# Optimization experiments

Hardware: AMD Instinct MI355X
Metric: run time of the kernel (lower is better)

## Reference

```python
import jax, jax.numpy as jnp
import numpy as np
from functools import partial

ALPHA = 2.0  # surrogate sharpness

@partial(jax.custom_vjp, nondiff_argnums=(1,))
def spike(x, alpha):
    # Heaviside forward, atan surrogate backward
    return (x >= 0.0).astype(x.dtype)

def _spike_fwd(x, alpha):
    return spike(x, alpha), x

def _spike_bwd(alpha, x, g):
    grad = (alpha / 2.0) / (1.0 + (jnp.pi / 2.0 * alpha * x) ** 2)
    return (g * grad,)

spike.defvjp(_spike_fwd, _spike_bwd)


def setup_inputs() -> dict:
    key = jax.random.key(0)
    k1, k2, k3 = jax.random.split(key, 3)
    B, T, H = 128, 2048, 512
    TAU_INIT, TH_INIT = 8.0, 0.5
    x_seq = jax.random.normal(k1, (B, T, 2), dtype=jnp.float32)
    W_in = jax.random.normal(k2, (2, H), dtype=jnp.float32) * (1.0 / np.sqrt(2.0))
    b_in = jnp.zeros((H,), dtype=jnp.float32)
    # PLIF: sigmoid(w_tau) = 1/tau  =>  w_tau = -log(tau - 1)
    w_tau = jnp.full((H,), -np.log(TAU_INIT - 1.0), dtype=jnp.float32)
    threshold = jnp.full((H,), TH_INIT, dtype=jnp.float32)
    W_out = jax.random.normal(k3, (H, 2), dtype=jnp.float32) * (1.0 / np.sqrt(H))
    b_out = jnp.zeros((2,), dtype=jnp.float32)
    return {"x_seq": x_seq, "W_in": W_in, "b_in": b_in,
            "w_tau": w_tau, "threshold": threshold,
            "W_out": W_out, "b_out": b_out}


def reference(x_seq, W_in, b_in, w_tau, threshold, W_out, b_out):
    B, T, _ = x_seq.shape
    H = W_in.shape[1]
    cur = x_seq @ W_in + b_in                      # [B, T, H]
    decay = jax.nn.sigmoid(w_tau)                  # [H], = 1/tau

    def step(v, c):
        v = v + (c - v) * decay                    # leaky integration
        s = spike(v - threshold, ALPHA)            # threshold + surrogate
        v = v * (1.0 - s)                          # hard reset
        return v, s

    v0 = jnp.zeros((B, H), dtype=x_seq.dtype)
    _, s_seq = jax.lax.scan(step, v0, jnp.transpose(cur, (1, 0, 2)))  # s_seq: [T, B, H]
    rate = s_seq.mean(axis=0)                      # [B, H]
    return rate @ W_out + b_out                    # [B, 2]
```

## Files before the change

### kernel.cpp

```cpp
#include <hip/hip_runtime.h>
#include <math.h>

#define NB 128
#define NT 2048
#define NH 512
#define HBLK 64
#define HCHUNKS 8
#define NCH 4
#define WARM 128
#define MAIN (NT / NCH)
#define WB (WARM / 8)
#define MB (MAIN / 8)

#define STEP2(q, CNT)                                             \
    do {                                                          \
        float cd1 = fmaf((q).x, A0, fmaf((q).y, A1, Bd));         \
        float vn1 = fmaf(vp, K, cd1);                             \
        vp = sp ? cd1 : vn1;                                      \
        sp = (vp >= th);                                          \
        if (CNT) cnt += sp ? 1 : 0;                               \
        float cd2 = fmaf((q).z, A0, fmaf((q).w, A1, Bd));         \
        float vn2 = fmaf(vp, K, cd2);                             \
        vp = sp ? cd2 : vn2;                                      \
        sp = (vp >= th);                                          \
        if (CNT) cnt += sp ? 1 : 0;                               \
    } while (0)

#define PROC8(q0, q1, q2, q3, CNT)                                \
    do {                                                          \
        STEP2(q0, CNT); STEP2(q1, CNT);                           \
        STEP2(q2, CNT); STEP2(q3, CNT);                           \
    } while (0)

__global__ __launch_bounds__(HBLK, 4)
void snn_scan_kernel(const float* __restrict__ x,
                     const float* __restrict__ W_in,
                     const float* __restrict__ b_in,
                     const float* __restrict__ w_tau,
                     const float* __restrict__ thr_p,
                     const float* __restrict__ W_out,
                     const float* __restrict__ b_out,
                     float* __restrict__ out) {
    const int blk = blockIdx.x;
    const int c   = blk & (NCH - 1);
    const int hc  = (blk >> 2) & (HCHUNKS - 1);
    const int b   = blk >> 5;
    const int h   = hc * HBLK + threadIdx.x;

    const float w0 = W_in[h];
    const float w1 = W_in[NH + h];
    const float bi = b_in[h];
    const float wt = w_tau[h];
    const float decay = (wt >= 0.0f)
        ? (1.0f / (1.0f + expf(-wt)))
        : ({ float e = expf(wt); e / (1.0f + e); });
    const float th = thr_p[h];

    const float A0 = w0 * decay;
    const float A1 = w1 * decay;
    const float Bd = bi * decay;
    const float K  = 1.0f - decay;

    int vz;
    asm volatile("v_mov_b32 %0, 0" : "=v"(vz));

    const int warm = c ? WARM : 0;
    const int wb   = c ? WB : 0;
    const int nb   = wb + MB;
    const int start_t = c * MAIN - warm;
    const float4* __restrict__ base =
        (const float4*)(x + (size_t)b * (NT * 2)) + (start_t >> 1);

#define LD(idx) base[(idx) + vz]

    float vp = 0.0f;
    bool  sp = false;
    int   cnt = 0;

    float4 a0 = LD(0), a1 = LD(1), a2 = LD(2), a3 = LD(3);
    float4 b0 = LD(4), b1 = LD(5), b2 = LD(6), b3 = LD(7);

    int i = 0;
    #pragma unroll 2
    for (; i < wb; ++i) {
        const int nx = (i + 2) * 4;
        float4 n0 = LD(nx), n1 = LD(nx + 1), n2 = LD(nx + 2), n3 = LD(nx + 3);
        PROC8(a0, a1, a2, a3, 0);
        a0 = b0; a1 = b1; a2 = b2; a3 = b3;
        b0 = n0; b1 = n1; b2 = n2; b3 = n3;
    }
    #pragma unroll 2
    for (; i < nb - 2; ++i) {
        const int nx = (i + 2) * 4;
        float4 n0 = LD(nx), n1 = LD(nx + 1), n2 = LD(nx + 2), n3 = LD(nx + 3);
        PROC8(a0, a1, a2, a3, 1);
        a0 = b0; a1 = b1; a2 = b2; a3 = b3;
        b0 = n0; b1 = n1; b2 = n2; b3 = n3;
    }
    PROC8(a0, a1, a2, a3, 1);
    PROC8(b0, b1, b2, b3, 1);
#undef LD

    float rate = (float)cnt * (1.0f / (float)NT);
    float o0 = rate * W_out[2 * h];
    float o1 = rate * W_out[2 * h + 1];

    #pragma unroll
    for (int off = 32; off > 0; off >>= 1) {
        o0 += __shfl_down(o0, off, 64);
        o1 += __shfl_down(o1, off, 64);
    }
    if (threadIdx.x == 0) {
        if (hc == 0 && c == 0) {
            o0 += b_out[0];
            o1 += b_out[1];
        }
        atomicAdd(&out[b * 2 + 0], o0);
        atomicAdd(&out[b * 2 + 1], o1);
    }
}

extern "C" void kernel_launch(void* const* d_in, const int* in_sizes, int n_in,
                              void* d_out, int out_size, void* d_ws, size_t ws_size,
                              hipStream_t stream) {
    const float* x     = (const float*)d_in[0];
    const float* W_in  = (const float*)d_in[1];
    const float* b_in  = (const float*)d_in[2];
    const float* w_tau = (const float*)d_in[3];
    const float* thr   = (const float*)d_in[4];
    const float* W_out = (const float*)d_in[5];
    const float* b_out = (const float*)d_in[6];
    float* out = (float*)d_out;

    hipMemsetAsync(out, 0, (size_t)out_size * sizeof(float), stream);
    hipLaunchKernelGGL(snn_scan_kernel,
                       dim3(NB * HCHUNKS * NCH), dim3(HBLK), 0, stream,
                       x, W_in, b_in, w_tau, thr, W_out, b_out, out);
}
```

Before: 119.5 us.

## Stage per-batch input chunk in shared memory with 512-thread blocks

Each block now covers all 512 hidden units of one batch and time chunk instead of 64, and loads that chunk's input sequence (with warm-up) into LDS once. The scan then reads inputs from shared memory rather than each wave issuing redundant global float4 loads. For chunk 0 the warm-up loop is run on the main data and the state is reset afterward, which adds wasted work in those blocks. It adds a block-wide barrier and uses fewer, larger blocks, which can change occupancy and latency hiding.

```diff
diff --git a/kernel.cpp b/kernel.cpp
--- a/kernel.cpp
+++ b/kernel.cpp
@@ -4,13 +4,12 @@
 #define NB 128
 #define NT 2048
 #define NH 512
-#define HBLK 64
-#define HCHUNKS 8
+#define HBLK 512
 #define NCH 4
 #define WARM 128
 #define MAIN (NT / NCH)
-#define WB (WARM / 8)
-#define MB (MAIN / 8)
+#define WB4 (WARM / 4)
+#define MB4 (MAIN / 4)
 
 #define STEP2(q, CNT)                                             \
     do {                                                          \
@@ -26,11 +25,7 @@
         if (CNT) cnt += sp ? 1 : 0;                               \
     } while (0)
 
-#define PROC8(q0, q1, q2, q3, CNT)                                \
-    do {                                                          \
-        STEP2(q0, CNT); STEP2(q1, CNT);                           \
-        STEP2(q2, CNT); STEP2(q3, CNT);                           \
-    } while (0)
+#define PROC4(p, r, CNT) do { STEP2(p, CNT); STEP2(r, CNT); } while (0)
 
 __global__ __launch_bounds__(HBLK, 4)
 void snn_scan_kernel(const float* __restrict__ x,
@@ -41,11 +36,21 @@
                      const float* __restrict__ W_out,
                      const float* __restrict__ b_out,
                      float* __restrict__ out) {
-    const int blk = blockIdx.x;
-    const int c   = blk & (NCH - 1);
-    const int hc  = (blk >> 2) & (HCHUNKS - 1);
-    const int b   = blk >> 5;
-    const int h   = hc * HBLK + threadIdx.x;
+    __shared__ float4 xs[320];
+
+    const int blk  = blockIdx.x;
+    const int c    = blk & (NCH - 1);
+    const int b    = blk >> 2;
+    const int tid  = threadIdx.x;
+    const int lane = tid & 63;
+    const int wv   = tid >> 6;
+    const int h    = wv * 64 + lane;
+
+    const int n4 = c ? 320 : 256;
+    const int s4 = c ? ((c * MAIN - WARM) >> 1) : 0;
+    const float4* __restrict__ src =
+        (const float4*)(x + (size_t)b * (NT * 2)) + s4;
+    if (tid < n4) xs[tid] = src[tid];
 
     const float w0 = W_in[h];
     const float w1 = W_in[NH + h];
@@ -61,45 +66,37 @@
     const float Bd = bi * decay;
     const float K  = 1.0f - decay;
 
-    int vz;
-    asm volatile("v_mov_b32 %0, 0" : "=v"(vz));
-
-    const int warm = c ? WARM : 0;
-    const int wb   = c ? WB : 0;
-    const int nb   = wb + MB;
-    const int start_t = c * MAIN - warm;
-    const float4* __restrict__ base =
-        (const float4*)(x + (size_t)b * (NT * 2)) + (start_t >> 1);
-
-#define LD(idx) base[(idx) + vz]
+    __syncthreads();
 
     float vp = 0.0f;
     bool  sp = false;
     int   cnt = 0;
 
-    float4 a0 = LD(0), a1 = LD(1), a2 = LD(2), a3 = LD(3);
-    float4 b0 = LD(4), b1 = LD(5), b2 = LD(6), b3 = LD(7);
+    const int mbase = c ? (WARM / 2) : 0;
 
-    int i = 0;
-    #pragma unroll 2
-    for (; i < wb; ++i) {
-        const int nx = (i + 2) * 4;
-        float4 n0 = LD(nx), n1 = LD(nx + 1), n2 = LD(nx + 2), n3 = LD(nx + 3);
-        PROC8(a0, a1, a2, a3, 0);
-        a0 = b0; a1 = b1; a2 = b2; a3 = b3;
-        b0 = n0; b1 = n1; b2 = n2; b3 = n3;
+    float4 p0 = xs[0], p1 = xs[1];
+    #pragma unroll 4
+    for (int i = 0; i < WB4 - 1; ++i) {
+        const int nx = 2 * (i + 1);
+        float4 n0 = xs[nx], n1 = xs[nx + 1];
+        PROC4(p0, p1, 0);
+        p0 = n0; p1 = n1;
     }
-    #pragma unroll 2
-    for (; i < nb - 2; ++i) {
-        const int nx = (i + 2) * 4;
-        float4 n0 = LD(nx), n1 = LD(nx + 1), n2 = LD(nx + 2), n3 = LD(nx + 3);
-        PROC8(a0, a1, a2, a3, 1);
-        a0 = b0; a1 = b1; a2 = b2; a3 = b3;
-        b0 = n0; b1 = n1; b2 = n2; b3 = n3;
+    {
+        float4 n0 = xs[mbase], n1 = xs[mbase + 1];
+        PROC4(p0, p1, 0);
+        p0 = n0; p1 = n1;
     }
-    PROC8(a0, a1, a2, a3, 1);
-    PROC8(b0, b1, b2, b3, 1);
-#undef LD
+    if (c == 0) { vp = 0.0f; sp = false; }
+
+    #pragma unroll 4
+    for (int i = 0; i < MB4 - 1; ++i) {
+        const int nx = mbase + 2 * (i + 1);
+        float4 n0 = xs[nx], n1 = xs[nx + 1];
+        PROC4(p0, p1, 1);
+        p0 = n0; p1 = n1;
+    }
+    PROC4(p0, p1, 1);
 
     float rate = (float)cnt * (1.0f / (float)NT);
     float o0 = rate * W_out[2 * h];
@@ -110,8 +107,8 @@
         o0 += __shfl_down(o0, off, 64);
         o1 += __shfl_down(o1, off, 64);
     }
-    if (threadIdx.x == 0) {
-        if (hc == 0 && c == 0) {
+    if (lane == 0) {
+        if (wv == 0 && c == 0) {
             o0 += b_out[0];
             o1 += b_out[1];
         }
@@ -134,6 +131,6 @@
 
     hipMemsetAsync(out, 0, (size_t)out_size * sizeof(float), stream);
     hipLaunchKernelGGL(snn_scan_kernel,
-                       dim3(NB * HCHUNKS * NCH), dim3(HBLK), 0, stream,
+                       dim3(NB * NCH), dim3(HBLK), 0, stream,
                        x, W_in, b_in, w_tau, thr, W_out, b_out, out);
 }
```

Result: faster. 96.75 us (-19.1%).
